# Performance work log

Hardware: AMD Instinct MI355X
Metric: run time of the kernel (lower is better)

The kernel has to match this reference:

```python
import jax, jax.numpy as jnp
import numpy as np

B = 8          # batch (one decode token per sequence)
H = 16         # query heads
HKV = 8        # kv heads (GQA)
G = H // HKV   # query heads per kv head
D = 128        # head_dim
HID = H * D    # 2048 hidden
VOCAB = 32000
BS = 16        # block_size
MAXB = 256     # blocks per sequence
NBLK = B * MAXB  # total cache blocks
L = MAXB * BS    # max context length = 4096


def setup_inputs() -> dict:
    key = jax.random.key(0)
    ks = jax.random.split(key, 12)
    w = 0.02
    return {
        "tokens": jax.random.randint(ks[0], (B,), 0, VOCAB),
        "positions": jax.random.randint(ks[1], (B,), 0, L - 1),
        "block_table": jnp.arange(B * MAXB, dtype=jnp.int32).reshape(B, MAXB),
        "k_cache": jax.random.normal(ks[2], (NBLK, BS, HKV, D), jnp.float32),
        "v_cache": jax.random.normal(ks[3], (NBLK, BS, HKV, D), jnp.float32),
        "embed": jax.random.normal(ks[4], (VOCAB, HID), jnp.float32) * w,
        "Wq": jax.random.normal(ks[5], (HID, HID), jnp.float32) * w,
        "Wk": jax.random.normal(ks[6], (HID, HKV * D), jnp.float32) * w,
        "Wv": jax.random.normal(ks[7], (HID, HKV * D), jnp.float32) * w,
        "Wo": jax.random.normal(ks[8], (HID, HID), jnp.float32) * w,
        "Wlm": jax.random.normal(ks[9], (HID, VOCAB), jnp.float32) * w,
    }


def reference(tokens, positions, block_table, k_cache, v_cache,
              embed, Wq, Wk, Wv, Wo, Wlm):
    # embed + projections for the single new token per sequence
    xf = embed[tokens]                                   # [B, HID]
    q = (xf @ Wq).reshape(B, HKV, G, D)                  # grouped-query layout
    k_new = (xf @ Wk).reshape(B, HKV, D)
    v_new = (xf @ Wv).reshape(B, HKV, D)

    # paged cache update: scatter new k/v into block_table[b, pos//BS] at offset pos%BS
    slot = block_table[jnp.arange(B), positions // BS] * BS + positions % BS  # [B]
    kc = k_cache.reshape(NBLK * BS, HKV, D).at[slot].set(k_new)
    vc = v_cache.reshape(NBLK * BS, HKV, D).at[slot].set(v_new)

    # paged decode: gather each sequence's KV via its block table
    idx = (block_table[:, :, None] * BS + jnp.arange(BS)[None, None, :]).reshape(B, L)
    kg = kc[idx]                                         # [B, L, HKV, D]
    vg = vc[idx]                                         # [B, L, HKV, D]

    scale = 1.0 / jnp.sqrt(jnp.float32(D))
    scores = jnp.einsum('bgcd,blgd->bgcl', q, kg) * scale  # [B, HKV, G, L]
    valid = jnp.arange(L)[None, :] <= positions[:, None]   # cache_seqlens + 1 tokens valid
    scores = jnp.where(valid[:, None, None, :], scores, -jnp.inf)
    attn = jax.nn.softmax(scores, axis=-1)
    attn_out = jnp.einsum('bgcl,blgd->bgcd', attn, vg).reshape(B, HID)

    out = attn_out @ Wo                                  # o_proj
    logits = (xf + out) @ Wlm                            # residual + lm_head
    return logits                                        # [B, VOCAB]
```

## Files before the change

### kernel.cpp

```cpp
#include <hip/hip_runtime.h>
#include <cstdint>
#include <cstddef>

constexpr int B_    = 8;
constexpr int HKV_  = 8;
constexpr int G_    = 2;
constexpr int D_    = 128;
constexpr int HID_  = 2048;
constexpr int VOCAB_= 32000;
constexpr int BS_   = 16;
constexpr int MAXB_ = 256;
constexpr int L_    = 4096;

constexpr int KSP_QKV = 32;  constexpr int CK_QKV = HID_ / KSP_QKV;
constexpr int KSP_O   = 32;
constexpr int KSP_LM  = 16;  constexpr int CK_LM  = HID_ / KSP_LM;
constexpr int CHUNK   = 128; constexpr int NCHUNK = L_ / CHUNK;
constexpr int NCOL_QKV = HID_ + 1024 + 1024;

constexpr size_t OFF_PQKV = 0;
constexpr size_t OFF_PM   = OFF_PQKV + (size_t)KSP_QKV*B_*NCOL_QKV;
constexpr size_t OFF_PL   = OFF_PM   + (size_t)B_*HKV_*NCHUNK*G_;
constexpr size_t OFF_PACC = OFF_PL   + (size_t)B_*HKV_*NCHUNK*G_;
constexpr size_t OFF_PO   = OFF_PACC + (size_t)B_*HKV_*NCHUNK*G_*D_;
constexpr size_t OFF_PLM  = OFF_PO   + (size_t)KSP_O*B_*HID_;

typedef float f32x4_t __attribute__((ext_vector_type(4)));
__device__ __forceinline__ float4 ntload4(const float* p) {
    f32x4_t v = __builtin_nontemporal_load((const f32x4_t*)p);
    return make_float4(v.x, v.y, v.z, v.w);
}
__device__ __forceinline__ float ntload1(const float* p) {
    return __builtin_nontemporal_load(p);
}

__global__ __launch_bounds__(256) void k_qkv_part(const int* __restrict__ tokens,
        const float* __restrict__ embed,
        const float* __restrict__ Wq, const float* __restrict__ Wk,
        const float* __restrict__ Wv, float* __restrict__ pout) {
    __shared__ float xs[CK_QKV * 8];
    const int c  = blockIdx.y;
    const int k0 = c * CK_QKV;
    const int n  = blockIdx.x * 256 + threadIdx.x;
    for (int idx = threadIdx.x; idx < CK_QKV*8; idx += 256) {
        int b = idx >> 6, kk = idx & (CK_QKV-1);
        xs[kk*8 + b] = embed[(size_t)tokens[b]*HID_ + k0 + kk];
    }
    const float* Wp; int stride, col;
    if (n < HID_)            { Wp = Wq; stride = HID_; col = n; }
    else if (n < HID_+1024)  { Wp = Wk; stride = 1024; col = n - HID_; }
    else                     { Wp = Wv; stride = 1024; col = n - HID_ - 1024; }
    __syncthreads();
    float acc[8] = {0,0,0,0,0,0,0,0};
    const float* wp = Wp + (size_t)k0 * stride + col;
    #pragma unroll 16
    for (int kk = 0; kk < CK_QKV; ++kk) {
        float w = ntload1(wp); wp += stride;
        float4 x0 = *(const float4*)&xs[kk*8];
        float4 x1 = *(const float4*)&xs[kk*8 + 4];
        acc[0] += x0.x*w; acc[1] += x0.y*w; acc[2] += x0.z*w; acc[3] += x0.w*w;
        acc[4] += x1.x*w; acc[5] += x1.y*w; acc[6] += x1.z*w; acc[7] += x1.w*w;
    }
    float* po = pout + (size_t)c * 8 * NCOL_QKV + n;
    #pragma unroll
    for (int b = 0; b < 8; ++b) po[(size_t)b*NCOL_QKV] = acc[b];
}

__global__ __launch_bounds__(256) void k_attn(const float* __restrict__ pqkv,
        const float* __restrict__ kc, const float* __restrict__ vc,
        const int* __restrict__ positions, const int* __restrict__ btab,
        float* __restrict__ pm, float* __restrict__ pl, float* __restrict__ pacc) {
    const int ch = blockIdx.x, hkv = blockIdx.y, b = blockIdx.z;
    const int pos = positions[b];
    const int c0  = ch * CHUNK;
    const size_t pbase = (size_t)(b*HKV_ + hkv)*NCHUNK + ch;
    const int t = threadIdx.x;
    if (c0 > pos) {
        if (t < 2) { pm[pbase*2 + t] = -1e30f; pl[pbase*2 + t] = 0.f; }
        pacc[pbase*256 + t] = 0.f;
        return;
    }
    const bool haspos = (pos < c0 + CHUNK);

    __shared__ float qs[2*D_];
    __shared__ float knvs[2*D_];
    __shared__ int   bts[CHUNK/BS_];
    __shared__ float acc_l[8][256];
    __shared__ float ml_l[8][2][2];

    const float4* pq4 = (const float4*)pqkv;
    const float scale = 0.08838834764831845f;
    if (t < 64) {
        float4 s = make_float4(0.f,0.f,0.f,0.f);
        size_t cb4 = (size_t)hkv*64 + t;
        for (int cc = 0; cc < KSP_QKV; ++cc) {
            float4 p = pq4[(size_t)(cc*8 + b)*(NCOL_QKV/4) + cb4];
            s.x += p.x; s.y += p.y; s.z += p.z; s.w += p.w;
        }
        s.x *= scale; s.y *= scale; s.z *= scale; s.w *= scale;
        ((float4*)qs)[t] = s;
    } else if (t < 128 && haspos) {
        int j = t - 64;
        size_t cb4 = (j < 32) ? (size_t)(HID_ + hkv*D_)/4 + j
                              : (size_t)(HID_ + 1024 + hkv*D_)/4 + (j - 32);
        float4 s = make_float4(0.f,0.f,0.f,0.f);
        for (int cc = 0; cc < KSP_QKV; ++cc) {
            float4 p = pq4[(size_t)(cc*8 + b)*(NCOL_QKV/4) + cb4];
            s.x += p.x; s.y += p.y; s.z += p.z; s.w += p.w;
        }
        ((float4*)knvs)[j] = s;
    }
    if (t < CHUNK/BS_) bts[t] = btab[b*MAXB_ + ch*(CHUNK/BS_) + t];
    __syncthreads();

    const int hw = t >> 5, l32 = t & 31;
    float4 q0 = ((const float4*)qs)[l32];
    float4 q1 = ((const float4*)qs)[32 + l32];

    float m0 = -1e30f, m1 = -1e30f, l0 = 0.f, l1 = 0.f;
    float a0[4] = {0,0,0,0}, a1[4] = {0,0,0,0};

    #pragma unroll 8
    for (int i = 0; i < CHUNK/8; ++i) {
        const int lo = i*8 + hw;
        const int l  = c0 + lo;
        const bool valid = (l < pos);
        size_t row = (size_t)bts[lo >> 4] * BS_ + (lo & (BS_-1));
        size_t off = (row*HKV_ + hkv)*D_ + l32*4;
        float4 kv = ntload4(kc + off);
        float4 vv = ntload4(vc + off);
        float s0 = q0.x*kv.x + q0.y*kv.y + q0.z*kv.z + q0.w*kv.w;
        float s1 = q1.x*kv.x + q1.y*kv.y + q1.z*kv.z + q1.w*kv.w;
        #pragma unroll
        for (int m = 16; m >= 1; m >>= 1) { s0 += __shfl_xor(s0, m); s1 += __shfl_xor(s1, m); }
        if (!valid) { s0 = -1e30f; s1 = -1e30f; }
        float nm0 = fmaxf(m0, s0);
        float cr0 = __expf(m0 - nm0);
        float p0  = valid ? __expf(s0 - nm0) : 0.f;
        m0 = nm0; l0 = l0*cr0 + p0;
        a0[0] = a0[0]*cr0 + p0*vv.x; a0[1] = a0[1]*cr0 + p0*vv.y;
        a0[2] = a0[2]*cr0 + p0*vv.z; a0[3] = a0[3]*cr0 + p0*vv.w;
        float nm1 = fmaxf(m1, s1);
        float cr1 = __expf(m1 - nm1);
        float p1  = valid ? __expf(s1 - nm1) : 0.f;
        m1 = nm1; l1 = l1*cr1 + p1;
        a1[0] = a1[0]*cr1 + p1*vv.x; a1[1] = a1[1]*cr1 + p1*vv.y;
        a1[2] = a1[2]*cr1 + p1*vv.z; a1[3] = a1[3]*cr1 + p1*vv.w;
    }

    if (haspos && hw == 0) {
        float4 kv = ((const float4*)knvs)[l32];
        float4 vv = ((const float4*)knvs)[32 + l32];
        float s0 = q0.x*kv.x + q0.y*kv.y + q0.z*kv.z + q0.w*kv.w;
        float s1 = q1.x*kv.x + q1.y*kv.y + q1.z*kv.z + q1.w*kv.w;
        #pragma unroll
        for (int m = 16; m >= 1; m >>= 1) { s0 += __shfl_xor(s0, m); s1 += __shfl_xor(s1, m); }
        float nm0 = fmaxf(m0, s0);
        float cr0 = __expf(m0 - nm0);
        float p0  = __expf(s0 - nm0);
        m0 = nm0; l0 = l0*cr0 + p0;
        a0[0] = a0[0]*cr0 + p0*vv.x; a0[1] = a0[1]*cr0 + p0*vv.y;
        a0[2] = a0[2]*cr0 + p0*vv.z; a0[3] = a0[3]*cr0 + p0*vv.w;
        float nm1 = fmaxf(m1, s1);
        float cr1 = __expf(m1 - nm1);
        float p1  = __expf(s1 - nm1);
        m1 = nm1; l1 = l1*cr1 + p1;
        a1[0] = a1[0]*cr1 + p1*vv.x; a1[1] = a1[1]*cr1 + p1*vv.y;
        a1[2] = a1[2]*cr1 + p1*vv.z; a1[3] = a1[3]*cr1 + p1*vv.w;
    }

    *(float4*)&acc_l[hw][0*D_ + l32*4] = make_float4(a0[0],a0[1],a0[2],a0[3]);
    *(float4*)&acc_l[hw][1*D_ + l32*4] = make_float4(a1[0],a1[1],a1[2],a1[3]);
    if (l32 == 0) {
        ml_l[hw][0][0] = m0; ml_l[hw][0][1] = l0;
        ml_l[hw][1][0] = m1; ml_l[hw][1][1] = l1;
    }
    __syncthreads();

    const int g = t >> 7, d = t & 127;
    float M = -1e30f;
    #pragma unroll
    for (int h = 0; h < 8; ++h) M = fmaxf(M, ml_l[h][g][0]);
    float Ls = 0.f, val = 0.f;
    #pragma unroll
    for (int h = 0; h < 8; ++h) {
        float w = __expf(ml_l[h][g][0] - M);
        Ls  += w * ml_l[h][g][1];
        val += w * acc_l[h][g*D_ + d];
    }
    pacc[pbase*256 + t] = val;
    if (d == 0) { pm[pbase*2 + g] = M; pl[pbase*2 + g] = Ls; }
}

__global__ __launch_bounds__(256) void k_o_part(const float* __restrict__ pm,
        const float* __restrict__ pl, const float* __restrict__ pacc,
        const float* __restrict__ Wo, float* __restrict__ po) {
    const int cb   = blockIdx.y;
    const int head = cb >> 1;
    const int hkv  = head >> 1, g = head & 1;
    const int dhalf = (cb & 1) * 64;
    const int t = threadIdx.x;
    const int n = blockIdx.x * 256 + t;

    __shared__ float pms[8][NCHUNK], pls[8][NCHUNK];
    __shared__ float wch[8][NCHUNK];
    __shared__ float wsum[8];
    __shared__ float xs[64 * 8];

    {
        int bb = t >> 5, ch = t & 31;
        size_t ix = ((size_t)(bb*HKV_ + hkv)*NCHUNK + ch)*2 + g;
        pms[bb][ch] = pm[ix];
        pls[bb][ch] = pl[ix];
    }
    __syncthreads();
    if (t < 8) {
        float M = -1e30f;
        for (int ch = 0; ch < NCHUNK; ++ch) M = fmaxf(M, pms[t][ch]);
        float Ls = 0.f;
        for (int ch = 0; ch < NCHUNK; ++ch) {
            float w = __expf(pms[t][ch] - M);
            wch[t][ch] = w;
            Ls += w * pls[t][ch];
        }
        wsum[t] = 1.f / Ls;
    }
    __syncthreads();
    if (t < 128) {
        int bb = t >> 4, j = t & 15;
        float4 a = make_float4(0.f,0.f,0.f,0.f);
        size_t base4 = ((size_t)(bb*HKV_ + hkv)*NCHUNK)*64 + (size_t)(g*128 + dhalf)/4 + j;
        for (int ch = 0; ch < NCHUNK; ++ch) {
            float w = wch[bb][ch];
            float4 p = ((const float4*)pacc)[base4 + (size_t)ch*64];
            a.x += w*p.x; a.y += w*p.y; a.z += w*p.z; a.w += w*p.w;
        }
        float inv = wsum[bb];
        xs[(j*4+0)*8 + bb] = a.x*inv;
        xs[(j*4+1)*8 + bb] = a.y*inv;
        xs[(j*4+2)*8 + bb] = a.z*inv;
        xs[(j*4+3)*8 + bb] = a.w*inv;
    }
    __syncthreads();

    float acc[8] = {0,0,0,0,0,0,0,0};
    const float* wp = Wo + (size_t)(head*D_ + dhalf) * HID_ + n;
    #pragma unroll 16
    for (int kk = 0; kk < 64; ++kk) {
        float w = ntload1(wp); wp += HID_;
        float4 x0 = *(const float4*)&xs[kk*8];
        float4 x1 = *(const float4*)&xs[kk*8 + 4];
        acc[0] += x0.x*w; acc[1] += x0.y*w; acc[2] += x0.z*w; acc[3] += x0.w*w;
        acc[4] += x1.x*w; acc[5] += x1.y*w; acc[6] += x1.z*w; acc[7] += x1.w*w;
    }
    #pragma unroll
    for (int b = 0; b < 8; ++b) po[((size_t)cb*8 + b)*HID_ + n] = acc[b];
}

__global__ __launch_bounds__(256) void k_lm_part(const int* __restrict__ tokens,
        const float* __restrict__ embed, const float* __restrict__ po,
        const float* __restrict__ Wlm, float* __restrict__ plm) {
    __shared__ float xs[CK_LM * 8];
    const int c  = blockIdx.y;
    const int k0 = c * CK_LM;
    const int t  = threadIdx.x;
    {
        int bb = t >> 5, j = t & 31;
        size_t col4 = (size_t)(k0 >> 2) + j;
        float4 a = ((const float4*)embed)[(size_t)tokens[bb]*(HID_/4) + col4];
        for (int c2 = 0; c2 < KSP_O; ++c2) {
            float4 p = ((const float4*)po)[(size_t)(c2*8 + bb)*(HID_/4) + col4];
            a.x += p.x; a.y += p.y; a.z += p.z; a.w += p.w;
        }
        xs[(j*4+0)*8 + bb] = a.x;
        xs[(j*4+1)*8 + bb] = a.y;
        xs[(j*4+2)*8 + bb] = a.z;
        xs[(j*4+3)*8 + bb] = a.w;
    }
    __syncthreads();

    const int n0 = blockIdx.x * 1024 + t * 4;
    if (n0 >= VOCAB_) return;
    float4 acc[8];
    #pragma unroll
    for (int b = 0; b < 8; ++b) acc[b] = make_float4(0.f,0.f,0.f,0.f);
    const float* wp = Wlm + (size_t)k0 * VOCAB_ + n0;
    #pragma unroll 8
    for (int kk = 0; kk < CK_LM; ++kk) {
        float4 w = *(const float4*)wp; wp += VOCAB_;
        float4 x0 = *(const float4*)&xs[kk*8];
        float4 x1 = *(const float4*)&xs[kk*8 + 4];
        acc[0].x += x0.x*w.x; acc[0].y += x0.x*w.y; acc[0].z += x0.x*w.z; acc[0].w += x0.x*w.w;
        acc[1].x += x0.y*w.x; acc[1].y += x0.y*w.y; acc[1].z += x0.y*w.z; acc[1].w += x0.y*w.w;
        acc[2].x += x0.z*w.x; acc[2].y += x0.z*w.y; acc[2].z += x0.z*w.z; acc[2].w += x0.z*w.w;
        acc[3].x += x0.w*w.x; acc[3].y += x0.w*w.y; acc[3].z += x0.w*w.z; acc[3].w += x0.w*w.w;
        acc[4].x += x1.x*w.x; acc[4].y += x1.x*w.y; acc[4].z += x1.x*w.z; acc[4].w += x1.x*w.w;
        acc[5].x += x1.y*w.x; acc[5].y += x1.y*w.y; acc[5].z += x1.y*w.z; acc[5].w += x1.y*w.w;
        acc[6].x += x1.z*w.x; acc[6].y += x1.z*w.y; acc[6].z += x1.z*w.z; acc[6].w += x1.z*w.w;
        acc[7].x += x1.w*w.x; acc[7].y += x1.w*w.y; acc[7].z += x1.w*w.z; acc[7].w += x1.w*w.w;
    }
    #pragma unroll
    for (int b = 0; b < 8; ++b)
        *(float4*)&plm[(size_t)(c*8 + b)*VOCAB_ + n0] = acc[b];
}

__global__ __launch_bounds__(256) void k_lm_comb(const float* __restrict__ plm,
                                                 float* __restrict__ out) {
    const int b = blockIdx.y;
    const int n4 = blockIdx.x * 256 + threadIdx.x;
    if (n4 >= VOCAB_/4) return;
    float4 s = make_float4(0.f,0.f,0.f,0.f);
    #pragma unroll
    for (int c = 0; c < KSP_LM; ++c) {
        float4 p = ((const float4*)plm)[(size_t)(c*8 + b)*(VOCAB_/4) + n4];
        s.x += p.x; s.y += p.y; s.z += p.z; s.w += p.w;
    }
    ((float4*)out)[(size_t)b*(VOCAB_/4) + n4] = s;
}

extern "C" void kernel_launch(void* const* d_in, const int* in_sizes, int n_in,
                              void* d_out, int out_size, void* d_ws, size_t ws_size,
                              hipStream_t stream) {
    const int*   tokens    = (const int*)  d_in[0];
    const int*   positions = (const int*)  d_in[1];
    const int*   btab      = (const int*)  d_in[2];
    const float* kc        = (const float*)d_in[3];
    const float* vc        = (const float*)d_in[4];
    const float* embed     = (const float*)d_in[5];
    const float* Wq        = (const float*)d_in[6];
    const float* Wk        = (const float*)d_in[7];
    const float* Wv        = (const float*)d_in[8];
    const float* Wo        = (const float*)d_in[9];
    const float* Wlm       = (const float*)d_in[10];
    float* out = (float*)d_out;
    float* ws  = (float*)d_ws;

    float* pqkv = ws + OFF_PQKV;
    float* pm   = ws + OFF_PM;
    float* pl   = ws + OFF_PL;
    float* pacc = ws + OFF_PACC;
    float* po   = ws + OFF_PO;
    float* plm  = ws + OFF_PLM;

    k_qkv_part<<<dim3(NCOL_QKV/256, KSP_QKV), 256, 0, stream>>>(tokens, embed, Wq, Wk, Wv, pqkv);
    k_attn    <<<dim3(NCHUNK, HKV_, B_), 256, 0, stream>>>(pqkv, kc, vc, positions, btab,
                                                           pm, pl, pacc);
    k_o_part  <<<dim3(HID_/256, KSP_O), 256, 0, stream>>>(pm, pl, pacc, Wo, po);
    k_lm_part <<<dim3((VOCAB_ + 1023)/1024, KSP_LM), 256, 0, stream>>>(tokens, embed, po, Wlm, plm);
    k_lm_comb <<<dim3((VOCAB_/4 + 255)/256, B_), 256, 0, stream>>>(plm, out);
}
```

Measured before the change: 112.1 us.

## Replace split-K partial buffers and combine kernel with atomic accumulation

The o_proj and lm_head split-K partial sums are now accumulated with float atomicAdd directly into a residual buffer y and into the output logits, instead of being written to workspace partial arrays and reduced later. The residual y is seeded with the embeddings in the QKV kernel, and the output is zeroed inside the o_proj kernel. This removes the k_lm_comb launch and the large partial-buffer writes and reads. In exchange it adds atomic contention (16 adds per logit, 32 per hidden element) and makes the floating-point summation order nondeterministic.

```diff
diff --git a/kernel.cpp b/kernel.cpp
--- a/kernel.cpp
+++ b/kernel.cpp
@@ -22,8 +22,7 @@
 constexpr size_t OFF_PM   = OFF_PQKV + (size_t)KSP_QKV*B_*NCOL_QKV;
 constexpr size_t OFF_PL   = OFF_PM   + (size_t)B_*HKV_*NCHUNK*G_;
 constexpr size_t OFF_PACC = OFF_PL   + (size_t)B_*HKV_*NCHUNK*G_;
-constexpr size_t OFF_PO   = OFF_PACC + (size_t)B_*HKV_*NCHUNK*G_*D_;
-constexpr size_t OFF_PLM  = OFF_PO   + (size_t)KSP_O*B_*HID_;
+constexpr size_t OFF_Y    = OFF_PACC + (size_t)B_*HKV_*NCHUNK*G_*D_;
 
 typedef float f32x4_t __attribute__((ext_vector_type(4)));
 __device__ __forceinline__ float4 ntload4(const float* p) {
@@ -37,7 +36,8 @@
 __global__ __launch_bounds__(256) void k_qkv_part(const int* __restrict__ tokens,
         const float* __restrict__ embed,
         const float* __restrict__ Wq, const float* __restrict__ Wk,
-        const float* __restrict__ Wv, float* __restrict__ pout) {
+        const float* __restrict__ Wv, float* __restrict__ pout,
+        float* __restrict__ y) {
     __shared__ float xs[CK_QKV * 8];
     const int c  = blockIdx.y;
     const int k0 = c * CK_QKV;
@@ -45,6 +45,11 @@
     for (int idx = threadIdx.x; idx < CK_QKV*8; idx += 256) {
         int b = idx >> 6, kk = idx & (CK_QKV-1);
         xs[kk*8 + b] = embed[(size_t)tokens[b]*HID_ + k0 + kk];
+    }
+    if (c == 0 && n < HID_) {
+        #pragma unroll
+        for (int b = 0; b < 8; ++b)
+            y[(size_t)b*HID_ + n] = embed[(size_t)tokens[b]*HID_ + n];
     }
     const float* Wp; int stride, col;
     if (n < HID_)            { Wp = Wq; stride = HID_; col = n; }
@@ -194,13 +199,20 @@
 
 __global__ __launch_bounds__(256) void k_o_part(const float* __restrict__ pm,
         const float* __restrict__ pl, const float* __restrict__ pacc,
-        const float* __restrict__ Wo, float* __restrict__ po) {
+        const float* __restrict__ Wo, float* __restrict__ y,
+        float* __restrict__ out) {
     const int cb   = blockIdx.y;
     const int head = cb >> 1;
     const int hkv  = head >> 1, g = head & 1;
     const int dhalf = (cb & 1) * 64;
     const int t = threadIdx.x;
     const int n = blockIdx.x * 256 + t;
+
+    {
+        int zid = (cb * gridDim.x + blockIdx.x) * 256 + t;
+        if (zid < (VOCAB_*B_)/4)
+            ((float4*)out)[zid] = make_float4(0.f,0.f,0.f,0.f);
+    }
 
     __shared__ float pms[8][NCHUNK], pls[8][NCHUNK];
     __shared__ float wch[8][NCHUNK];
@@ -254,24 +266,18 @@
         acc[4] += x1.x*w; acc[5] += x1.y*w; acc[6] += x1.z*w; acc[7] += x1.w*w;
     }
     #pragma unroll
-    for (int b = 0; b < 8; ++b) po[((size_t)cb*8 + b)*HID_ + n] = acc[b];
-}
-
-__global__ __launch_bounds__(256) void k_lm_part(const int* __restrict__ tokens,
-        const float* __restrict__ embed, const float* __restrict__ po,
-        const float* __restrict__ Wlm, float* __restrict__ plm) {
+    for (int b = 0; b < 8; ++b) atomicAdd(&y[(size_t)b*HID_ + n], acc[b]);
+}
+
+__global__ __launch_bounds__(256) void k_lm_part(const float* __restrict__ y,
+        const float* __restrict__ Wlm, float* __restrict__ out) {
     __shared__ float xs[CK_LM * 8];
     const int c  = blockIdx.y;
     const int k0 = c * CK_LM;
     const int t  = threadIdx.x;
     {
         int bb = t >> 5, j = t & 31;
-        size_t col4 = (size_t)(k0 >> 2) + j;
-        float4 a = ((const float4*)embed)[(size_t)tokens[bb]*(HID_/4) + col4];
-        for (int c2 = 0; c2 < KSP_O; ++c2) {
-            float4 p = ((const float4*)po)[(size_t)(c2*8 + bb)*(HID_/4) + col4];
-            a.x += p.x; a.y += p.y; a.z += p.z; a.w += p.w;
-        }
+        float4 a = ((const float4*)y)[(size_t)bb*(HID_/4) + (k0 >> 2) + j];
         xs[(j*4+0)*8 + bb] = a.x;
         xs[(j*4+1)*8 + bb] = a.y;
         xs[(j*4+2)*8 + bb] = a.z;
@@ -300,22 +306,13 @@
         acc[7].x += x1.w*w.x; acc[7].y += x1.w*w.y; acc[7].z += x1.w*w.z; acc[7].w += x1.w*w.w;
     }
     #pragma unroll
-    for (int b = 0; b < 8; ++b)
-        *(float4*)&plm[(size_t)(c*8 + b)*VOCAB_ + n0] = acc[b];
-}
-
-__global__ __launch_bounds__(256) void k_lm_comb(const float* __restrict__ plm,
-                                                 float* __restrict__ out) {
-    const int b = blockIdx.y;
-    const int n4 = blockIdx.x * 256 + threadIdx.x;
-    if (n4 >= VOCAB_/4) return;
-    float4 s = make_float4(0.f,0.f,0.f,0.f);
-    #pragma unroll
-    for (int c = 0; c < KSP_LM; ++c) {
-        float4 p = ((const float4*)plm)[(size_t)(c*8 + b)*(VOCAB_/4) + n4];
-        s.x += p.x; s.y += p.y; s.z += p.z; s.w += p.w;
-    }
-    ((float4*)out)[(size_t)b*(VOCAB_/4) + n4] = s;
+    for (int b = 0; b < 8; ++b) {
+        float* op = out + (size_t)b*VOCAB_ + n0;
+        atomicAdd(op + 0, acc[b].x);
+        atomicAdd(op + 1, acc[b].y);
+        atomicAdd(op + 2, acc[b].z);
+        atomicAdd(op + 3, acc[b].w);
+    }
 }
 
 extern "C" void kernel_launch(void* const* d_in, const int* in_sizes, int n_in,
@@ -339,13 +336,12 @@
     float* pm   = ws + OFF_PM;
     float* pl   = ws + OFF_PL;
     float* pacc = ws + OFF_PACC;
-    float* po   = ws + OFF_PO;
-    float* plm  = ws + OFF_PLM;
-
-    k_qkv_part<<<dim3(NCOL_QKV/256, KSP_QKV), 256, 0, stream>>>(tokens, embed, Wq, Wk, Wv, pqkv);
+    float* y    = ws + OFF_Y;
+
+    k_qkv_part<<<dim3(NCOL_QKV/256, KSP_QKV), 256, 0, stream>>>(tokens, embed, Wq, Wk, Wv,
+                                                                pqkv, y);
     k_attn    <<<dim3(NCHUNK, HKV_, B_), 256, 0, stream>>>(pqkv, kc, vc, positions, btab,
                                                            pm, pl, pacc);
-    k_o_part  <<<dim3(HID_/256, KSP_O), 256, 0, stream>>>(pm, pl, pacc, Wo, po);
-    k_lm_part <<<dim3((VOCAB_ + 1023)/1024, KSP_LM), 256, 0, stream>>>(tokens, embed, po, Wlm, plm);
-    k_lm_comb <<<dim3((VOCAB_/4 + 255)/256, B_), 256, 0, stream>>>(plm, out);
-}
+    k_o_part  <<<dim3(HID_/256, KSP_O), 256, 0, stream>>>(pm, pl, pacc, Wo, y, out);
+    k_lm_part <<<dim3((VOCAB_ + 1023)/1024, KSP_LM), 256, 0, stream>>>(y, Wlm, out);
+}
```

Measured after the change: 146.8 us. 1.31x slower.
